# Performance work log

Hardware: AMD Instinct MI355X
Metric: run time of the kernel (lower is better)

Reference implementation:

```python
import jax, jax.numpy as jnp
import numpy as np

EPS = 1e-5

def setup_inputs() -> dict:
    key = jax.random.key(0)
    k1, k2, k3 = jax.random.split(key, 3)
    B, T, F = 64, 512, 1024
    x = jax.random.normal(k1, (B, T, F), dtype=jnp.float32)
    # Linear(width_time, width_time): torch stores weight as (out, in)
    W = jax.random.normal(k2, (T, T), dtype=jnp.float32) * (1.0 / np.sqrt(T))
    b = jax.random.normal(k3, (T,), dtype=jnp.float32) * 0.01
    gamma = jnp.ones((1,), dtype=jnp.float32)
    beta = jnp.zeros((1,), dtype=jnp.float32)
    return {"x": x, "W": W, "b": b, "gamma": gamma, "beta": beta}


def reference(x, W, b, gamma, beta):
    # TSBatchNorm2d: BatchNorm2d(num_features=1) over x.unsqueeze(1)
    # -> stats over all (B, T, F) elements, scalar affine (training-mode batch stats).
    mean = jnp.mean(x)
    var = jnp.var(x)
    y = (x - mean) * jax.lax.rsqrt(var + EPS) * gamma[0] + beta[0]
    # transpose (B,T,F) -> (B,F,T), Linear over time dim, ReLU
    # (dropout is identity in eval mode), transpose back, residual add.
    yt = jnp.swapaxes(y, 1, 2)                      # (B, F, T)
    h = jnp.einsum('bft,ut->bfu', yt, W) + b        # Linear: y @ W.T + b
    h = jax.nn.relu(h)
    return x + jnp.swapaxes(h, 1, 2)                # (B, T, F)
```

## Files before the change

kernel.cpp:

```cpp
#include <hip/hip_runtime.h>
#include <stdint.h>

#define TDIM 512
#define FDIM 1024
#define NTOT 33554432.0f
#define EPS  1e-5f

typedef unsigned short ushort_t;
typedef unsigned short ushort4_t __attribute__((ext_vector_type(4)));
typedef short short8 __attribute__((ext_vector_type(8)));
typedef float floatx4 __attribute__((ext_vector_type(4)));

__device__ __forceinline__ ushort_t f2bf(float f) {
    union { float f; uint32_t u; } v; v.f = f;
    uint32_t r = (v.u + 0x7fffu + ((v.u >> 16) & 1u)) >> 16;
    return (ushort_t)r;
}

__device__ __forceinline__ void async16(const ushort_t* g, ushort_t* l) {
    __builtin_amdgcn_global_load_lds(
        (const __attribute__((address_space(1))) void*)g,
        (__attribute__((address_space(3))) void*)l, 16, 0, 0);
}

__global__ __launch_bounds__(256) void k_stats_transpose(
    const float* __restrict__ x, ushort_t* __restrict__ xT,
    float2* __restrict__ partials)
{
    __shared__ ushort_t tile[128 * 68];
    __shared__ float red[8];

    int tid = threadIdx.x;
    int bid = blockIdx.x;
    int b   = bid >> 6;
    int t0  = ((bid >> 3) & 7) << 6;
    int f0  = (bid & 7) << 7;

    int r8 = tid >> 5, c8 = tid & 31;
    const float* xb = x + ((size_t)(b * TDIM + t0) * FDIM) + f0;

    float4 v[8];
#pragma unroll
    for (int p = 0; p < 8; ++p)
        v[p] = *(const float4*)(xb + (size_t)(p * 8 + r8) * FDIM + c8 * 4);

    float s = 0.f, q = 0.f;
#pragma unroll
    for (int p = 0; p < 8; ++p) {
        float4 t = v[p];
        s += t.x + t.y + t.z + t.w;
        q += t.x * t.x + t.y * t.y + t.z * t.z + t.w * t.w;
        int row = p * 8 + r8;
        int fl  = c8 * 4;
        tile[(fl + 0) * 68 + row] = f2bf(t.x);
        tile[(fl + 1) * 68 + row] = f2bf(t.y);
        tile[(fl + 2) * 68 + row] = f2bf(t.z);
        tile[(fl + 3) * 68 + row] = f2bf(t.w);
    }

#pragma unroll
    for (int off = 32; off > 0; off >>= 1) {
        s += __shfl_down(s, off, 64);
        q += __shfl_down(q, off, 64);
    }
    int lane = tid & 63, w = tid >> 6;
    if (lane == 0) { red[w] = s; red[4 + w] = q; }
    __syncthreads();
    if (tid == 0) {
        partials[bid] = make_float2(red[0] + red[1] + red[2] + red[3],
                                    red[4] + red[5] + red[6] + red[7]);
    }

    int fr = tid >> 1, half = tid & 1;
    ushort_t* dst = xT + ((size_t)(b * FDIM + f0 + fr) * TDIM) + t0 + half * 32;
    const ushort_t* srcp = &tile[fr * 68 + half * 32];
#pragma unroll
    for (int k = 0; k < 8; ++k)
        *(ushort4_t*)(dst + k * 4) = *(const ushort4_t*)(srcp + k * 4);
}

__global__ __launch_bounds__(256) void k_wcast(
    const float* __restrict__ W, ushort_t* __restrict__ Wb,
    float* __restrict__ rowsumW)
{
    __shared__ float red[4];
    int u = blockIdx.x, tid = threadIdx.x;
    const float* row = W + (size_t)u * 512;
    float v0 = row[tid], v1 = row[tid + 256];
    Wb[u * 512 + tid]       = f2bf(v0);
    Wb[u * 512 + tid + 256] = f2bf(v1);
    float s = v0 + v1;
#pragma unroll
    for (int off = 32; off > 0; off >>= 1) s += __shfl_down(s, off, 64);
    int lane = tid & 63, w = tid >> 6;
    if (lane == 0) red[w] = s;
    __syncthreads();
    if (tid == 0) rowsumW[u] = red[0] + red[1] + red[2] + red[3];
}

__global__ __launch_bounds__(256) void k_reduce(
    const float2* __restrict__ partials, const float* __restrict__ rowsumW,
    const float* __restrict__ bias, const float* __restrict__ gamma,
    const float* __restrict__ beta, float* __restrict__ stats,
    float* __restrict__ d)
{
    __shared__ float red[8];
    __shared__ float sac[2];
    int tid = threadIdx.x;
    float s = 0.f, q = 0.f;
#pragma unroll
    for (int i = 0; i < 16; ++i) {
        float2 p = partials[i * 256 + tid];
        s += p.x; q += p.y;
    }
#pragma unroll
    for (int off = 32; off > 0; off >>= 1) {
        s += __shfl_down(s, off, 64);
        q += __shfl_down(q, off, 64);
    }
    int lane = tid & 63, w = tid >> 6;
    if (lane == 0) { red[w] = s; red[4 + w] = q; }
    __syncthreads();
    if (tid == 0) {
        float S = red[0] + red[1] + red[2] + red[3];
        float Q = red[4] + red[5] + red[6] + red[7];
        float mean = S * (1.f / NTOT);
        float var  = Q * (1.f / NTOT) - mean * mean;
        float a    = gamma[0] * rsqrtf(var + EPS);
        float c    = beta[0] - mean * a;
        stats[0] = a;
        sac[0] = a; sac[1] = c;
    }
    __syncthreads();
    float c = sac[1];
    d[tid]       = c * rowsumW[tid]       + bias[tid];
    d[tid + 256] = c * rowsumW[tid + 256] + bias[tid + 256];
}

__global__ __launch_bounds__(256) void k_gemm(
    const ushort_t* __restrict__ Wb, const ushort_t* __restrict__ xT,
    const float* __restrict__ x, const float* __restrict__ d,
    const float* __restrict__ stats, float* __restrict__ out)
{
    __shared__ ushort_t ldsA[4096];
    __shared__ ushort_t ldsB[4096];

    int tid = threadIdx.x;
    int w = tid >> 6, lane = tid & 63;
    int mt = blockIdx.x;
    int nt = blockIdx.y;
    int b = nt >> 3, ft = nt & 7;
    int wr = w >> 1, wc = w & 1;
    int l15 = lane & 15, q = lane >> 4;

    const ushort_t* Abase = Wb + (size_t)(mt * 128) * 512;
    const ushort_t* Bbase = xT + ((size_t)b * FDIM + ft * 128) * 512;

    floatx4 acc[4][4] = {};

    for (int kt = 0; kt < 512; kt += 32) {
#pragma unroll
        for (int c = 0; c < 2; ++c) {
            int ci = c * 256 + tid;
            int qs = ci >> 7, is = ci & 127;
            async16(Abase + (size_t)is * 512 + kt + qs * 8, &ldsA[ci * 8]);
            async16(Bbase + (size_t)is * 512 + kt + qs * 8, &ldsB[ci * 8]);
        }
        __syncthreads();

        short8 af[4], bfr[4];
#pragma unroll
        for (int i = 0; i < 4; ++i) {
            int m = wr * 64 + i * 16 + l15;
            af[i] = *(const short8*)&ldsA[(q * 128 + m) * 8];
        }
#pragma unroll
        for (int j = 0; j < 4; ++j) {
            int n = wc * 64 + j * 16 + l15;
            bfr[j] = *(const short8*)&ldsB[(q * 128 + n) * 8];
        }
#pragma unroll
        for (int i = 0; i < 4; ++i)
#pragma unroll
            for (int j = 0; j < 4; ++j)
                acc[i][j] = __builtin_amdgcn_mfma_f32_16x16x32_bf16(
                    af[i], bfr[j], acc[i][j], 0, 0, 0);
        __syncthreads();
    }

    float a = stats[0];
#pragma unroll
    for (int i = 0; i < 4; ++i) {
#pragma unroll
        for (int r = 0; r < 4; ++r) {
            int t = mt * 128 + wr * 64 + i * 16 + q * 4 + r;
            float dt = d[t];
            size_t rowbase = ((size_t)b * TDIM + t) * FDIM + ft * 128 + wc * 64 + l15;
#pragma unroll
            for (int j = 0; j < 4; ++j) {
                size_t idx = rowbase + j * 16;
                float h = a * acc[i][j][r] + dt;
                out[idx] = x[idx] + fmaxf(h, 0.f);
            }
        }
    }
}

extern "C" void kernel_launch(void* const* d_in, const int* in_sizes, int n_in,
                              void* d_out, int out_size, void* d_ws, size_t ws_size,
                              hipStream_t stream) {
    const float* x     = (const float*)d_in[0];
    const float* W     = (const float*)d_in[1];
    const float* bias  = (const float*)d_in[2];
    const float* gamma = (const float*)d_in[3];
    const float* beta  = (const float*)d_in[4];
    float* out = (float*)d_out;

    char* ws = (char*)d_ws;
    float*    stats    = (float*)ws;
    float*    dvec     = (float*)(ws + 1024);
    float*    rowsumW  = (float*)(ws + 4096);
    float2*   partials = (float2*)(ws + 8192);
    ushort_t* Wb       = (ushort_t*)(ws + (64 << 10));
    ushort_t* xT       = (ushort_t*)(ws + (1 << 20));

    k_stats_transpose<<<4096, 256, 0, stream>>>(x, xT, partials);
    k_wcast<<<512, 256, 0, stream>>>(W, Wb, rowsumW);
    k_reduce<<<1, 256, 0, stream>>>(partials, rowsumW, bias, gamma, beta, stats, dvec);
    k_gemm<<<dim3(4, 512), 256, 0, stream>>>(Wb, xT, x, dvec, stats, out);
}
```

Measured before the change: 343.6 us.

## Pre-tile GEMM operands into LDS-ready chunks and stage epilogue through LDS

```diff
diff --git a/kernel.cpp b/kernel.cpp
--- a/kernel.cpp
+++ b/kernel.cpp
@@ -23,18 +23,19 @@
         (__attribute__((address_space(3))) void*)l, 16, 0, 0);
 }
 
+
 __global__ __launch_bounds__(256) void k_stats_transpose(
-    const float* __restrict__ x, ushort_t* __restrict__ xT,
+    const float* __restrict__ x, ushort_t* __restrict__ xTC,
     float2* __restrict__ partials)
 {
-    __shared__ ushort_t tile[128 * 68];
+    __shared__ ushort_t tile[64 * 128];
     __shared__ float red[8];
 
-    int tid = threadIdx.x;
-    int bid = blockIdx.x;
-    int b   = bid >> 6;
-    int t0  = ((bid >> 3) & 7) << 6;
-    int f0  = (bid & 7) << 7;
+    int tid = threadIdx.x, bid = blockIdx.x;
+    int b  = bid >> 6;
+    int t0 = ((bid >> 3) & 7) << 6;
+    int ft = bid & 7;
+    int f0 = ft << 7;
 
     int r8 = tid >> 5, c8 = tid & 31;
     const float* xb = x + ((size_t)(b * TDIM + t0) * FDIM) + f0;
@@ -50,12 +51,9 @@
         float4 t = v[p];
         s += t.x + t.y + t.z + t.w;
         q += t.x * t.x + t.y * t.y + t.z * t.z + t.w * t.w;
-        int row = p * 8 + r8;
-        int fl  = c8 * 4;
-        tile[(fl + 0) * 68 + row] = f2bf(t.x);
-        tile[(fl + 1) * 68 + row] = f2bf(t.y);
-        tile[(fl + 2) * 68 + row] = f2bf(t.z);
-        tile[(fl + 3) * 68 + row] = f2bf(t.w);
+        ushort4_t pk;
+        pk[0] = f2bf(t.x); pk[1] = f2bf(t.y); pk[2] = f2bf(t.z); pk[3] = f2bf(t.w);
+        *(ushort4_t*)&tile[(p * 8 + r8) * 128 + c8 * 4] = pk;
     }
 
 #pragma unroll
@@ -71,27 +69,39 @@
                                     red[4] + red[5] + red[6] + red[7]);
     }
 
-    int fr = tid >> 1, half = tid & 1;
-    ushort_t* dst = xT + ((size_t)(b * FDIM + f0 + fr) * TDIM) + t0 + half * 32;
-    const ushort_t* srcp = &tile[fr * 68 + half * 32];
-#pragma unroll
-    for (int k = 0; k < 8; ++k)
-        *(ushort4_t*)(dst + k * 4) = *(const ushort4_t*)(srcp + k * 4);
+    int fl = tid & 127, hf = tid >> 7;
+    size_t base = ((size_t)((b * 8 + ft) * 16) + (t0 >> 5) + hf) * 4096;
+#pragma unroll
+    for (int qq = 0; qq < 4; ++qq) {
+        int tr = hf * 32 + qq * 8;
+        uint32_t w0 = (uint32_t)tile[(tr + 0) * 128 + fl] | ((uint32_t)tile[(tr + 1) * 128 + fl] << 16);
+        uint32_t w1 = (uint32_t)tile[(tr + 2) * 128 + fl] | ((uint32_t)tile[(tr + 3) * 128 + fl] << 16);
+        uint32_t w2 = (uint32_t)tile[(tr + 4) * 128 + fl] | ((uint32_t)tile[(tr + 5) * 128 + fl] << 16);
+        uint32_t w3 = (uint32_t)tile[(tr + 6) * 128 + fl] | ((uint32_t)tile[(tr + 7) * 128 + fl] << 16);
+        uint4 o = make_uint4(w0, w1, w2, w3);
+        *(uint4*)&xTC[base + (size_t)(qq * 128 + fl) * 8] = o;
+    }
 }
 
 __global__ __launch_bounds__(256) void k_wcast(
-    const float* __restrict__ W, ushort_t* __restrict__ Wb,
+    const float* __restrict__ W, ushort_t* __restrict__ WbC,
     float* __restrict__ rowsumW)
 {
     __shared__ float red[4];
     int u = blockIdx.x, tid = threadIdx.x;
-    const float* row = W + (size_t)u * 512;
-    float v0 = row[tid], v1 = row[tid + 256];
-    Wb[u * 512 + tid]       = f2bf(v0);
-    Wb[u * 512 + tid + 256] = f2bf(v1);
-    float s = v0 + v1;
-#pragma unroll
-    for (int off = 32; off > 0; off >>= 1) s += __shfl_down(s, off, 64);
+    float2 lv = *(const float2*)(W + (size_t)u * 512 + 2 * tid);
+
+    int mt = u >> 7, m = u & 127;
+    int kt = tid >> 4;
+    int qq = (tid & 15) >> 2;
+    int e  = 2 * (tid & 3);
+    size_t off = ((size_t)(mt * 16 + kt)) * 4096 + (size_t)(qq * 128 + m) * 8 + e;
+    uint32_t pk = (uint32_t)f2bf(lv.x) | ((uint32_t)f2bf(lv.y) << 16);
+    *(uint32_t*)&WbC[off] = pk;
+
+    float s = lv.x + lv.y;
+#pragma unroll
+    for (int off2 = 32; off2 > 0; off2 >>= 1) s += __shfl_down(s, off2, 64);
     int lane = tid & 63, w = tid >> 6;
     if (lane == 0) red[w] = s;
     __syncthreads();
@@ -138,12 +148,14 @@
 }
 
 __global__ __launch_bounds__(256) void k_gemm(
-    const ushort_t* __restrict__ Wb, const ushort_t* __restrict__ xT,
+    const ushort_t* __restrict__ WbC, const ushort_t* __restrict__ xTC,
     const float* __restrict__ x, const float* __restrict__ d,
     const float* __restrict__ stats, float* __restrict__ out)
 {
-    __shared__ ushort_t ldsA[4096];
-    __shared__ ushort_t ldsB[4096];
+    __shared__ ulong smem_raw[2176];
+    ushort_t* ldsA = (ushort_t*)smem_raw;
+    ushort_t* ldsB = ldsA + 4096;
+    float*    ldsC = (float*)smem_raw;
 
     int tid = threadIdx.x;
     int w = tid >> 6, lane = tid & 63;
@@ -153,19 +165,18 @@
     int wr = w >> 1, wc = w & 1;
     int l15 = lane & 15, q = lane >> 4;
 
-    const ushort_t* Abase = Wb + (size_t)(mt * 128) * 512;
-    const ushort_t* Bbase = xT + ((size_t)b * FDIM + ft * 128) * 512;
+    const ushort_t* Abase = WbC + (size_t)mt * 16 * 4096;
+    const ushort_t* Bbase = xTC + (size_t)(b * 8 + ft) * 16 * 4096;
 
     floatx4 acc[4][4] = {};
 
-    for (int kt = 0; kt < 512; kt += 32) {
-#pragma unroll
-        for (int c = 0; c < 2; ++c) {
-            int ci = c * 256 + tid;
-            int qs = ci >> 7, is = ci & 127;
-            async16(Abase + (size_t)is * 512 + kt + qs * 8, &ldsA[ci * 8]);
-            async16(Bbase + (size_t)is * 512 + kt + qs * 8, &ldsB[ci * 8]);
-        }
+    for (int kt = 0; kt < 16; ++kt) {
+        const ushort_t* Ag = Abase + kt * 4096 + tid * 8;
+        const ushort_t* Bg = Bbase + kt * 4096 + tid * 8;
+        async16(Ag,        &ldsA[tid * 8]);
+        async16(Ag + 2048, &ldsA[2048 + tid * 8]);
+        async16(Bg,        &ldsB[tid * 8]);
+        async16(Bg + 2048, &ldsB[2048 + tid * 8]);
         __syncthreads();
 
         short8 af[4], bfr[4];
@@ -189,20 +200,41 @@
     }
 
     float a = stats[0];
-#pragma unroll
-    for (int i = 0; i < 4; ++i) {
-#pragma unroll
-        for (int r = 0; r < 4; ++r) {
-            int t = mt * 128 + wr * 64 + i * 16 + q * 4 + r;
-            float dt = d[t];
-            size_t rowbase = ((size_t)b * TDIM + t) * FDIM + ft * 128 + wc * 64 + l15;
-#pragma unroll
-            for (int j = 0; j < 4; ++j) {
-                size_t idx = rowbase + j * 16;
-                float h = a * acc[i][j][r] + dt;
-                out[idx] = x[idx] + fmaxf(h, 0.f);
+    int row = tid >> 3, cs = (tid & 7) * 16;
+#pragma unroll
+    for (int p = 0; p < 4; ++p) {
+        if (wr == (p >> 1)) {
+#pragma unroll
+            for (int ii = 0; ii < 2; ++ii) {
+                int i = (p & 1) * 2 + ii;
+                int rl0 = i * 16 + q * 4 - (p & 1) * 32;
+#pragma unroll
+                for (int j = 0; j < 4; ++j) {
+                    int col = wc * 64 + j * 16 + l15;
+#pragma unroll
+                    for (int r = 0; r < 4; ++r)
+                        ldsC[(rl0 + r) * 132 + col] = acc[i][j][r];
+                }
             }
         }
+        __syncthreads();
+        int tg = mt * 128 + p * 32 + row;
+        float dt = d[tg];
+        size_t gbase = ((size_t)b * TDIM + tg) * FDIM + ft * 128 + cs;
+        const float* xr = x + gbase;
+        float* orow = out + gbase;
+#pragma unroll
+        for (int k4 = 0; k4 < 4; ++k4) {
+            float4 xv = *(const float4*)(xr + k4 * 4);
+            float4 cv = *(const float4*)&ldsC[row * 132 + cs + k4 * 4];
+            float4 o;
+            o.x = xv.x + fmaxf(a * cv.x + dt, 0.f);
+            o.y = xv.y + fmaxf(a * cv.y + dt, 0.f);
+            o.z = xv.z + fmaxf(a * cv.z + dt, 0.f);
+            o.w = xv.w + fmaxf(a * cv.w + dt, 0.f);
+            *(float4*)(orow + k4 * 4) = o;
+        }
+        __syncthreads();
     }
 }
 
@@ -221,11 +253,11 @@
     float*    dvec     = (float*)(ws + 1024);
     float*    rowsumW  = (float*)(ws + 4096);
     float2*   partials = (float2*)(ws + 8192);
-    ushort_t* Wb       = (ushort_t*)(ws + (64 << 10));
-    ushort_t* xT       = (ushort_t*)(ws + (1 << 20));
-
-    k_stats_transpose<<<4096, 256, 0, stream>>>(x, xT, partials);
-    k_wcast<<<512, 256, 0, stream>>>(W, Wb, rowsumW);
+    ushort_t* WbC      = (ushort_t*)(ws + (64 << 10));
+    ushort_t* xTC      = (ushort_t*)(ws + (1 << 20));
+
+    k_stats_transpose<<<4096, 256, 0, stream>>>(x, xTC, partials);
+    k_wcast<<<512, 256, 0, stream>>>(W, WbC, rowsumW);
     k_reduce<<<1, 256, 0, stream>>>(partials, rowsumW, bias, gamma, beta, stats, dvec);
-    k_gemm<<<dim3(4, 512), 256, 0, stream>>>(Wb, xT, x, dvec, stats, out);
-}
+    k_gemm<<<dim3(4, 512), 256, 0, stream>>>(WbC, xTC, x, dvec, stats, out);
+}
```

Measured after the change: 327.7 us. 1.05x faster.
